# Kernel optimization log

Measured on AMD Instinct MI355X. Metric: run time of the kernel, lower is better.

## Reference

```python
import jax, jax.numpy as jnp
import numpy as np

T, B, I, H = 8192, 1, 1024, 1024


def _lstm_layer(x, W_ih, W_hh, b_ih, b_hh):
    # x: [T, B, I]; torch gate order: input, forget, cell(g), output
    Hh = W_hh.shape[1]
    xg = jnp.einsum('tbi,gi->tbg', x, W_ih) + b_ih + b_hh  # [T, B, 4H]

    def step(carry, xg_t):
        h, c = carry
        gates = xg_t + h @ W_hh.T  # [B, 4H]
        i, f, g, o = jnp.split(gates, 4, axis=-1)
        c = jax.nn.sigmoid(f) * c + jax.nn.sigmoid(i) * jnp.tanh(g)
        h = jax.nn.sigmoid(o) * jnp.tanh(c)
        return (h, c), h

    h0 = jnp.zeros((x.shape[1], Hh), x.dtype)
    (_, _), ys = jax.lax.scan(step, (h0, h0), xg)
    return ys  # [T, B, H]


def setup_inputs() -> dict:
    key = jax.random.key(0)
    ks = jax.random.split(key, 9)
    s = 0.02
    return {
        'inputs': jax.random.normal(ks[0], (T, B, I), dtype=jnp.float32),
        'W_ih0': jax.random.normal(ks[1], (4 * H, I), dtype=jnp.float32) * s,
        'W_hh0': jax.random.normal(ks[2], (4 * H, H), dtype=jnp.float32) * s,
        'b_ih0': jax.random.normal(ks[3], (4 * H,), dtype=jnp.float32) * s,
        'b_hh0': jax.random.normal(ks[4], (4 * H,), dtype=jnp.float32) * s,
        'W_ih1': jax.random.normal(ks[5], (4 * H, H), dtype=jnp.float32) * s,
        'W_hh1': jax.random.normal(ks[6], (4 * H, H), dtype=jnp.float32) * s,
        'b_ih1': jax.random.normal(ks[7], (4 * H,), dtype=jnp.float32) * s,
        'b_hh1': jax.random.normal(ks[8], (4 * H,), dtype=jnp.float32) * s,
    }


def reference(inputs, W_ih0, W_hh0, b_ih0, b_hh0, W_ih1, W_hh1, b_ih1, b_hh1):
    # 2-layer LSTM, zero initial state, dropout omitted (eval semantics)
    y0 = _lstm_layer(inputs, W_ih0, W_hh0, b_ih0, b_hh0)
    y1 = _lstm_layer(y0, W_ih1, W_hh1, b_ih1, b_hh1)
    return y1[-1]  # [B, H] — last timestep of top layer
```

## Files before the change

kernel.cpp:

```cpp
#include <hip/hip_runtime.h>

#define T_STEPS 8192
#define HID 1024
#define G4 4096
#define NBLK 128
#define NTHR 512

typedef unsigned long long ull;
typedef unsigned int uint32;

struct Comm {
    uint32 hA[4][HID];
    uint32 hB[4][HID];
};

__device__ inline float sigm(float x) { return 1.0f / (1.0f + __expf(-x)); }
__device__ inline float tanh_f(float x) {
    x = fminf(fmaxf(x, -15.f), 15.f);
    float e = __expf(-2.0f * x);
    return (1.0f - e) / (1.0f + e);
}
__device__ inline uint32 tagf(float f, uint32 tg) {
    union { float f; uint32 u; } a; a.f = f;
    return (a.u & ~15u) | tg;
}

__global__ __launch_bounds__(256)
void gemm_xg(const float* __restrict__ A, const float* __restrict__ W,
             const float* __restrict__ bi, const float* __restrict__ bh,
             float* __restrict__ out)
{
    __shared__ float As[16][65];
    __shared__ float Bs[16][65];
    const int tid = threadIdx.x;
    const int m0 = blockIdx.y * 64, n0 = blockIdx.x * 64;
    const int tm = tid & 15, tn = tid >> 4;
    const int row = tid >> 2, q = tid & 3;
    float acc[4][4] = {{0.f}};
    for (int k0 = 0; k0 < HID; k0 += 16) {
        float4 a = *(const float4*)(A + (size_t)(m0 + row) * HID + k0 + q * 4);
        float4 b = *(const float4*)(W + (size_t)(n0 + row) * HID + k0 + q * 4);
        __syncthreads();
        As[q*4+0][row] = a.x; As[q*4+1][row] = a.y; As[q*4+2][row] = a.z; As[q*4+3][row] = a.w;
        Bs[q*4+0][row] = b.x; Bs[q*4+1][row] = b.y; Bs[q*4+2][row] = b.z; Bs[q*4+3][row] = b.w;
        __syncthreads();
#pragma unroll
        for (int kk = 0; kk < 16; ++kk) {
            float av[4], bv[4];
#pragma unroll
            for (int i = 0; i < 4; ++i) { av[i] = As[kk][tm*4+i]; bv[i] = Bs[kk][tn*4+i]; }
#pragma unroll
            for (int i = 0; i < 4; ++i)
#pragma unroll
                for (int j = 0; j < 4; ++j) acc[i][j] += av[i] * bv[j];
        }
    }
#pragma unroll
    for (int i = 0; i < 4; ++i) {
        int m = m0 + tm * 4 + i;
#pragma unroll
        for (int j = 0; j < 4; ++j) {
            int n = n0 + tn * 4 + j;
            float v = acc[i][j] + bi[n] + bh[n];
            int jd = n & (HID - 1), gate = n >> 10;
            out[(size_t)m * G4 + (jd >> 3) * 32 + (jd & 7) * 4 + gate] = v;
        }
    }
}

__device__ inline void poll_gather(const uint32* __restrict__ buf, uint32 tg,
                                   int lane, float* __restrict__ lds)
{
    uint32 v[16];
    for (;;) {
        bool ok = true;
#pragma unroll
        for (int r = 0; r < 16; ++r)
            v[r] = __hip_atomic_load(&buf[lane + 64 * r],
                                     __ATOMIC_RELAXED, __HIP_MEMORY_SCOPE_AGENT);
#pragma unroll
        for (int r = 0; r < 16; ++r) ok &= ((v[r] & 15u) == tg);
        if (__all(ok)) break;
    }
#pragma unroll
    for (int r = 0; r < 16; ++r) {
        union { uint32 u; float f; } c; c.u = v[r];
        lds[lane + 64 * r] = c.f;
    }
}

__global__ __launch_bounds__(NTHR)
void lstm_fused(const float* __restrict__ Whh0, const float* __restrict__ xg,
                const float* __restrict__ Wih1, const float* __restrict__ Whh1,
                const float* __restrict__ bih1, const float* __restrict__ bhh1,
                float* __restrict__ outF, Comm* __restrict__ cm)
{
    __shared__ float Wl[32 * HID];
    __shared__ float hlA[HID];
    __shared__ float hlB[HID];
    const int blk = blockIdx.x, tid = threadIdx.x;
    const int wave = tid >> 6, lane = tid & 63;

    if (blk < NBLK) {
        const int k = blk;
#pragma unroll
        for (int i = 0; i < 16; ++i) {
            int l = i * NTHR + tid;
            int r = l >> 8, c = l & 255;
            int w = r >> 2, g = r & 3;
            ((float4*)(Wl + r * HID))[c] =
                ((const float4*)(Whh0 + (size_t)(g * HID + 8 * k + w) * HID))[c];
        }
        for (int i = tid; i < HID; i += NTHR) hlA[i] = 0.f;
        float c_state = 0.f;
        float nx0 = 0.f, nx1 = 0.f, nx2 = 0.f, nx3 = 0.f;
        if (lane == 0) {
            const float* xp = xg + (size_t)0 * G4 + k * 32 + wave * 4;
            nx0 = xp[0]; nx1 = xp[1]; nx2 = xp[2]; nx3 = xp[3];
        }
        __syncthreads();

        for (int t = 0; t < T_STEPS; ++t) {
            float x0 = nx0, x1 = nx1, x2 = nx2, x3 = nx3;
            if (lane == 0 && t + 1 < T_STEPS) {
                const float* xp = xg + (size_t)(t + 1) * G4 + k * 32 + wave * 4;
                nx0 = xp[0]; nx1 = xp[1]; nx2 = xp[2]; nx3 = xp[3];
            }
            float a0 = 0.f, a1 = 0.f, a2 = 0.f, a3 = 0.f;
            const float* wb = Wl + wave * 4 * HID;
#pragma unroll 4
            for (int u = 0; u < 16; ++u) {
                float hv = hlA[u * 64 + lane];
                a0 += wb[0 * HID + u * 64 + lane] * hv;
                a1 += wb[1 * HID + u * 64 + lane] * hv;
                a2 += wb[2 * HID + u * 64 + lane] * hv;
                a3 += wb[3 * HID + u * 64 + lane] * hv;
            }
#pragma unroll
            for (int off = 32; off > 0; off >>= 1) {
                a0 += __shfl_xor(a0, off, 64);
                a1 += __shfl_xor(a1, off, 64);
                a2 += __shfl_xor(a2, off, 64);
                a3 += __shfl_xor(a3, off, 64);
            }
            if (lane == 0) {
                float ig = sigm(x0 + a0);
                float fg = sigm(x1 + a1);
                float gg = tanh_f(x2 + a2);
                float og = sigm(x3 + a3);
                c_state = fg * c_state + ig * gg;
                float h = og * tanh_f(c_state);
                __hip_atomic_store(&cm->hA[t & 3][8 * k + wave],
                                   tagf(h, (t >> 2) & 15),
                                   __ATOMIC_RELAXED, __HIP_MEMORY_SCOPE_AGENT);
            }
            if (t == T_STEPS - 1) break;
            __syncthreads();
            if (wave == 0) {
                poll_gather(cm->hA[t & 3], (t >> 2) & 15, lane, hlA);
            } else if (wave == 1 && t >= 3) {
                const int s = t - 3;
                const uint32 tg = (s >> 2) & 15;
                const uint32* hb = cm->hB[s & 3];
                for (;;) {
                    uint32 b0 = __hip_atomic_load(&hb[8 * lane],
                                                  __ATOMIC_RELAXED, __HIP_MEMORY_SCOPE_AGENT);
                    uint32 b1 = __hip_atomic_load(&hb[8 * (lane + 64)],
                                                  __ATOMIC_RELAXED, __HIP_MEMORY_SCOPE_AGENT);
                    if (__all(((b0 & 15u) == tg) & ((b1 & 15u) == tg))) break;
                }
            }
            __syncthreads();
        }
    } else {
        const int kk = blk - NBLK;
        const int j = 8 * kk + wave;
#pragma unroll
        for (int i = 0; i < 16; ++i) {
            int l = i * NTHR + tid;
            int r = l >> 8, c = l & 255;
            int w = r >> 2, g = r & 3;
            ((float4*)(Wl + r * HID))[c] =
                ((const float4*)(Whh1 + (size_t)(g * HID + 8 * kk + w) * HID))[c];
        }
        float wreg[4][16];
#pragma unroll
        for (int g = 0; g < 4; ++g)
#pragma unroll
            for (int u = 0; u < 16; ++u)
                wreg[g][u] = Wih1[(size_t)(g * HID + j) * HID + u * 64 + lane];
        float bia[4];
#pragma unroll
        for (int g = 0; g < 4; ++g)
            bia[g] = bih1[g * HID + j] + bhh1[g * HID + j];
        for (int i = tid; i < HID; i += NTHR) hlB[i] = 0.f;
        float c_state = 0.f;
        __syncthreads();

        for (int t = 0; t < T_STEPS; ++t) {
            if (wave == 0) {
                poll_gather(cm->hA[t & 3], (t >> 2) & 15, lane, hlA);
            } else if (wave == 1 && t >= 1) {
                const int s = t - 1;
                poll_gather(cm->hB[s & 3], (s >> 2) & 15, lane, hlB);
            }
            __syncthreads();
            float a0 = 0.f, a1 = 0.f, a2 = 0.f, a3 = 0.f;
            const float* wb = Wl + wave * 4 * HID;
#pragma unroll
            for (int u = 0; u < 16; ++u) {
                float h0v = hlA[u * 64 + lane];
                float h1v = hlB[u * 64 + lane];
                a0 += wb[0 * HID + u * 64 + lane] * h1v + wreg[0][u] * h0v;
                a1 += wb[1 * HID + u * 64 + lane] * h1v + wreg[1][u] * h0v;
                a2 += wb[2 * HID + u * 64 + lane] * h1v + wreg[2][u] * h0v;
                a3 += wb[3 * HID + u * 64 + lane] * h1v + wreg[3][u] * h0v;
            }
#pragma unroll
            for (int off = 32; off > 0; off >>= 1) {
                a0 += __shfl_xor(a0, off, 64);
                a1 += __shfl_xor(a1, off, 64);
                a2 += __shfl_xor(a2, off, 64);
                a3 += __shfl_xor(a3, off, 64);
            }
            if (lane == 0) {
                float ig = sigm(bia[0] + a0);
                float fg = sigm(bia[1] + a1);
                float gg = tanh_f(bia[2] + a2);
                float og = sigm(bia[3] + a3);
                c_state = fg * c_state + ig * gg;
                float h = og * tanh_f(c_state);
                if (t == T_STEPS - 1) {
                    outF[j] = h;
                } else {
                    __hip_atomic_store(&cm->hB[t & 3][j],
                                       tagf(h, (t >> 2) & 15),
                                       __ATOMIC_RELAXED, __HIP_MEMORY_SCOPE_AGENT);
                }
            }
            if (t == T_STEPS - 1) break;
            __syncthreads();
        }
    }
}

extern "C" void kernel_launch(void* const* d_in, const int* in_sizes, int n_in,
                              void* d_out, int out_size, void* d_ws, size_t ws_size,
                              hipStream_t stream)
{
    const float* x    = (const float*)d_in[0];
    const float* Wih0 = (const float*)d_in[1];
    const float* Whh0 = (const float*)d_in[2];
    const float* bih0 = (const float*)d_in[3];
    const float* bhh0 = (const float*)d_in[4];
    const float* Wih1 = (const float*)d_in[5];
    const float* Whh1 = (const float*)d_in[6];
    const float* bih1 = (const float*)d_in[7];
    const float* bhh1 = (const float*)d_in[8];

    char* ws = (char*)d_ws;
    float* xg = (float*)ws;
    Comm*  cm = (Comm*)(ws + 134217728);

    (void)hipMemsetAsync(ws + 134217728, 0xFF, sizeof(Comm), stream);

    dim3 gg(G4 / 64, T_STEPS / 64);
    gemm_xg<<<gg, 256, 0, stream>>>(x, Wih0, bih0, bhh0, xg);
    lstm_fused<<<2 * NBLK, NTHR, 0, stream>>>(Whh0, xg, Wih1, Whh1, bih1, bhh1,
                                              (float*)d_out, cm);
}
```

Baseline: 41.64 ms.

## Replace block barriers with per-chunk LDS flags and streamed polling in fused LSTM

Removes the two __syncthreads per timestep in both layer blocks and replaces them with fine-grained workgroup-scope flags. Polling now publishes each 64-element chunk of h to LDS as soon as it arrives, so compute waves can start on early chunks. It also double-buffers the h LDS arrays, widens the global ring to 8 slots with progress counters for backpressure, and interleaves W in LDS so each lane reads one float4 per column. The cost is more spin-waiting on LDS flags and more complex memory-ordering logic, which risks subtle races or livelock.

```diff
diff --git a/kernel.cpp b/kernel.cpp
--- a/kernel.cpp
+++ b/kernel.cpp
@@ -5,13 +5,13 @@
 #define G4 4096
 #define NBLK 128
 #define NTHR 512
-
-typedef unsigned long long ull;
+#define NSLOT 8
+
 typedef unsigned int uint32;
 
 struct Comm {
-    uint32 hA[4][HID];
-    uint32 hB[4][HID];
+    uint32 hA[NSLOT][HID];
+    uint32 hB[NSLOT][HID];
 };
 
 __device__ inline float sigm(float x) { return 1.0f / (1.0f + __expf(-x)); }
@@ -68,24 +68,33 @@
     }
 }
 
-__device__ inline void poll_gather(const uint32* __restrict__ buf, uint32 tg,
-                                   int lane, float* __restrict__ lds)
+#define LD_WG  __HIP_MEMORY_SCOPE_WORKGROUP
+#define LD_AG  __HIP_MEMORY_SCOPE_AGENT
+
+__device__ inline void poll_stream(const uint32* __restrict__ buf, uint32 tg,
+                                   int lane, float* __restrict__ lds,
+                                   int* __restrict__ flags, int fval)
 {
     uint32 v[16];
-    for (;;) {
-        bool ok = true;
+    unsigned pending = 0xFFFFu;
+    while (pending) {
 #pragma unroll
         for (int r = 0; r < 16; ++r)
-            v[r] = __hip_atomic_load(&buf[lane + 64 * r],
-                                     __ATOMIC_RELAXED, __HIP_MEMORY_SCOPE_AGENT);
-#pragma unroll
-        for (int r = 0; r < 16; ++r) ok &= ((v[r] & 15u) == tg);
-        if (__all(ok)) break;
-    }
-#pragma unroll
-    for (int r = 0; r < 16; ++r) {
-        union { uint32 u; float f; } c; c.u = v[r];
-        lds[lane + 64 * r] = c.f;
+            if (pending & (1u << r))
+                v[r] = __hip_atomic_load(&buf[r * 64 + lane], __ATOMIC_RELAXED, LD_AG);
+        unsigned np = pending;
+#pragma unroll
+        for (int r = 0; r < 16; ++r) {
+            if (!(pending & (1u << r))) continue;
+            if (__all((v[r] & 15u) == tg)) {
+                union { uint32 u; float f; } c; c.u = v[r];
+                lds[r * 64 + lane] = c.f;
+                if (lane == 0)
+                    __hip_atomic_store(&flags[r], fval, __ATOMIC_RELEASE, LD_WG);
+                np &= ~(1u << r);
+            }
+        }
+        pending = np;
     }
 }
 
@@ -95,46 +104,62 @@
                 const float* __restrict__ bih1, const float* __restrict__ bhh1,
                 float* __restrict__ outF, Comm* __restrict__ cm)
 {
-    __shared__ float Wl[32 * HID];
-    __shared__ float hlA[HID];
-    __shared__ float hlB[HID];
+    __shared__ float Wl[8 * HID * 4];
+    __shared__ float hlA[2][HID];
+    __shared__ float hlB[2][HID];
+    __shared__ int flagA[2][16];
+    __shared__ int flagB[2][16];
+    __shared__ int prog[8];
+    __shared__ int bpOK;
     const int blk = blockIdx.x, tid = threadIdx.x;
     const int wave = tid >> 6, lane = tid & 63;
-
-    if (blk < NBLK) {
-        const int k = blk;
+    const int kb = (blk < NBLK) ? blk : blk - NBLK;
+
+    if (tid < 16) { flagA[0][tid] = -2; flagA[1][tid] = -1;
+                    flagB[0][tid] = -2; flagB[1][tid] = -1; }
+    if (tid < 8) prog[tid] = -1;
+    if (tid == 0) bpOK = -1;
+    for (int i = tid; i < HID; i += NTHR) {
+        hlA[0][i] = 0.f; hlA[1][i] = 0.f; hlB[0][i] = 0.f; hlB[1][i] = 0.f;
+    }
+    {
+        const float* Wsrc = (blk < NBLK) ? Whh0 : Whh1;
 #pragma unroll
         for (int i = 0; i < 16; ++i) {
             int l = i * NTHR + tid;
-            int r = l >> 8, c = l & 255;
+            int r = l >> 8, c4 = l & 255;
             int w = r >> 2, g = r & 3;
-            ((float4*)(Wl + r * HID))[c] =
-                ((const float4*)(Whh0 + (size_t)(g * HID + 8 * k + w) * HID))[c];
-        }
-        for (int i = tid; i < HID; i += NTHR) hlA[i] = 0.f;
+            float4 v = ((const float4*)(Wsrc + (size_t)(g * HID + 8 * kb + w) * HID))[c4];
+            float* dst = Wl + ((size_t)w * HID + c4 * 4) * 4 + g;
+            dst[0] = v.x; dst[4] = v.y; dst[8] = v.z; dst[12] = v.w;
+        }
+    }
+
+    if (blk < NBLK) {
+        const int k = kb;
         float c_state = 0.f;
         float nx0 = 0.f, nx1 = 0.f, nx2 = 0.f, nx3 = 0.f;
         if (lane == 0) {
-            const float* xp = xg + (size_t)0 * G4 + k * 32 + wave * 4;
+            const float* xp = xg + k * 32 + wave * 4;
             nx0 = xp[0]; nx1 = xp[1]; nx2 = xp[2]; nx3 = xp[3];
         }
         __syncthreads();
 
         for (int t = 0; t < T_STEPS; ++t) {
+            const int pm = (t - 1) & 1;
             float x0 = nx0, x1 = nx1, x2 = nx2, x3 = nx3;
             if (lane == 0 && t + 1 < T_STEPS) {
                 const float* xp = xg + (size_t)(t + 1) * G4 + k * 32 + wave * 4;
                 nx0 = xp[0]; nx1 = xp[1]; nx2 = xp[2]; nx3 = xp[3];
             }
             float a0 = 0.f, a1 = 0.f, a2 = 0.f, a3 = 0.f;
-            const float* wb = Wl + wave * 4 * HID;
-#pragma unroll 4
+            const float* wb = Wl + (size_t)wave * HID * 4;
+#pragma unroll
             for (int u = 0; u < 16; ++u) {
-                float hv = hlA[u * 64 + lane];
-                a0 += wb[0 * HID + u * 64 + lane] * hv;
-                a1 += wb[1 * HID + u * 64 + lane] * hv;
-                a2 += wb[2 * HID + u * 64 + lane] * hv;
-                a3 += wb[3 * HID + u * 64 + lane] * hv;
+                while (__hip_atomic_load(&flagA[pm][u], __ATOMIC_ACQUIRE, LD_WG) != t - 1) {}
+                float hv = hlA[pm][u * 64 + lane];
+                float4 wv = *(const float4*)(wb + (u * 64 + lane) * 4);
+                a0 += wv.x * hv; a1 += wv.y * hv; a2 += wv.z * hv; a3 += wv.w * hv;
             }
 #pragma unroll
             for (int off = 32; off > 0; off >>= 1) {
@@ -143,6 +168,7 @@
                 a2 += __shfl_xor(a2, off, 64);
                 a3 += __shfl_xor(a3, off, 64);
             }
+            while (__hip_atomic_load(&bpOK, __ATOMIC_RELAXED, LD_WG) < t - 7) {}
             if (lane == 0) {
                 float ig = sigm(x0 + a0);
                 float fg = sigm(x1 + a1);
@@ -150,39 +176,40 @@
                 float og = sigm(x3 + a3);
                 c_state = fg * c_state + ig * gg;
                 float h = og * tanh_f(c_state);
-                __hip_atomic_store(&cm->hA[t & 3][8 * k + wave],
-                                   tagf(h, (t >> 2) & 15),
-                                   __ATOMIC_RELAXED, __HIP_MEMORY_SCOPE_AGENT);
+                __hip_atomic_store(&cm->hA[t & 7][8 * k + wave],
+                                   tagf(h, (t >> 3) & 15), __ATOMIC_RELAXED, LD_AG);
             }
             if (t == T_STEPS - 1) break;
-            __syncthreads();
+
             if (wave == 0) {
-                poll_gather(cm->hA[t & 3], (t >> 2) & 15, lane, hlA);
-            } else if (wave == 1 && t >= 3) {
-                const int s = t - 3;
-                const uint32 tg = (s >> 2) & 15;
-                const uint32* hb = cm->hB[s & 3];
-                for (;;) {
-                    uint32 b0 = __hip_atomic_load(&hb[8 * lane],
-                                                  __ATOMIC_RELAXED, __HIP_MEMORY_SCOPE_AGENT);
-                    uint32 b1 = __hip_atomic_load(&hb[8 * (lane + 64)],
-                                                  __ATOMIC_RELAXED, __HIP_MEMORY_SCOPE_AGENT);
-                    if (__all(((b0 & 15u) == tg) & ((b1 & 15u) == tg))) break;
+                if (lane < 8)
+                    while (__hip_atomic_load(&prog[lane], __ATOMIC_ACQUIRE, LD_WG) < t - 1) {}
+                poll_stream(cm->hA[t & 7], (t >> 3) & 15, lane, hlA[t & 1], flagA[t & 1], t);
+                if (lane == 0) __hip_atomic_store(&prog[0], t, __ATOMIC_RELEASE, LD_WG);
+            } else if (wave == 1) {
+                if (t >= 6) {
+                    const int s = t - 6;
+                    const uint32 tg = (s >> 3) & 15;
+                    const uint32* hb = cm->hB[s & 7];
+                    uint32 v[16];
+                    for (;;) {
+                        bool ok = true;
+#pragma unroll
+                        for (int r = 0; r < 16; ++r)
+                            v[r] = __hip_atomic_load(&hb[r * 64 + lane], __ATOMIC_RELAXED, LD_AG);
+#pragma unroll
+                        for (int r = 0; r < 16; ++r) ok &= ((v[r] & 15u) == tg);
+                        if (__all(ok)) break;
+                    }
+                    if (lane == 0) __hip_atomic_store(&bpOK, s, __ATOMIC_RELEASE, LD_WG);
                 }
-            }
-            __syncthreads();
+                if (lane == 0) __hip_atomic_store(&prog[1], t, __ATOMIC_RELEASE, LD_WG);
+            } else {
+                if (lane == 0) __hip_atomic_store(&prog[wave], t, __ATOMIC_RELEASE, LD_WG);
+            }
         }
     } else {
-        const int kk = blk - NBLK;
-        const int j = 8 * kk + wave;
-#pragma unroll
-        for (int i = 0; i < 16; ++i) {
-            int l = i * NTHR + tid;
-            int r = l >> 8, c = l & 255;
-            int w = r >> 2, g = r & 3;
-            ((float4*)(Wl + r * HID))[c] =
-                ((const float4*)(Whh1 + (size_t)(g * HID + 8 * kk + w) * HID))[c];
-        }
+        const int j = 8 * kb + wave;
         float wreg[4][16];
 #pragma unroll
         for (int g = 0; g < 4; ++g)
@@ -193,28 +220,36 @@
 #pragma unroll
         for (int g = 0; g < 4; ++g)
             bia[g] = bih1[g * HID + j] + bhh1[g * HID + j];
-        for (int i = tid; i < HID; i += NTHR) hlB[i] = 0.f;
         float c_state = 0.f;
         __syncthreads();
 
         for (int t = 0; t < T_STEPS; ++t) {
+            const int pA = t & 1, pB = (t - 1) & 1;
             if (wave == 0) {
-                poll_gather(cm->hA[t & 3], (t >> 2) & 15, lane, hlA);
+                if (t >= 2 && lane < 8)
+                    while (__hip_atomic_load(&prog[lane], __ATOMIC_ACQUIRE, LD_WG) < t - 2) {}
+                poll_stream(cm->hA[t & 7], (t >> 3) & 15, lane, hlA[pA], flagA[pA], t);
             } else if (wave == 1 && t >= 1) {
-                const int s = t - 1;
-                poll_gather(cm->hB[s & 3], (s >> 2) & 15, lane, hlB);
-            }
-            __syncthreads();
+                if (t >= 3 && lane < 8)
+                    while (__hip_atomic_load(&prog[lane], __ATOMIC_ACQUIRE, LD_WG) < t - 2) {}
+                poll_stream(cm->hB[(t - 1) & 7], ((t - 1) >> 3) & 15, lane,
+                            hlB[pB], flagB[pB], t - 1);
+            }
             float a0 = 0.f, a1 = 0.f, a2 = 0.f, a3 = 0.f;
-            const float* wb = Wl + wave * 4 * HID;
+            const float* wb = Wl + (size_t)wave * HID * 4;
 #pragma unroll
             for (int u = 0; u < 16; ++u) {
-                float h0v = hlA[u * 64 + lane];
-                float h1v = hlB[u * 64 + lane];
-                a0 += wb[0 * HID + u * 64 + lane] * h1v + wreg[0][u] * h0v;
-                a1 += wb[1 * HID + u * 64 + lane] * h1v + wreg[1][u] * h0v;
-                a2 += wb[2 * HID + u * 64 + lane] * h1v + wreg[2][u] * h0v;
-                a3 += wb[3 * HID + u * 64 + lane] * h1v + wreg[3][u] * h0v;
+                while (__hip_atomic_load(&flagB[pB][u], __ATOMIC_ACQUIRE, LD_WG) != t - 1) {}
+                float hv = hlB[pB][u * 64 + lane];
+                float4 wv = *(const float4*)(wb + (u * 64 + lane) * 4);
+                a0 += wv.x * hv; a1 += wv.y * hv; a2 += wv.z * hv; a3 += wv.w * hv;
+            }
+#pragma unroll
+            for (int u = 0; u < 16; ++u) {
+                while (__hip_atomic_load(&flagA[pA][u], __ATOMIC_ACQUIRE, LD_WG) != t) {}
+                float hv = hlA[pA][u * 64 + lane];
+                a0 += wreg[0][u] * hv; a1 += wreg[1][u] * hv;
+                a2 += wreg[2][u] * hv; a3 += wreg[3][u] * hv;
             }
 #pragma unroll
             for (int off = 32; off > 0; off >>= 1) {
@@ -230,16 +265,15 @@
                 float og = sigm(bia[3] + a3);
                 c_state = fg * c_state + ig * gg;
                 float h = og * tanh_f(c_state);
-                if (t == T_STEPS - 1) {
+                if (t == T_STEPS - 1)
                     outF[j] = h;
-                } else {
-                    __hip_atomic_store(&cm->hB[t & 3][j],
-                                       tagf(h, (t >> 2) & 15),
-                                       __ATOMIC_RELAXED, __HIP_MEMORY_SCOPE_AGENT);
-                }
+                else
+                    __hip_atomic_store(&cm->hB[t & 7][j],
+                                       tagf(h, (t >> 3) & 15), __ATOMIC_RELAXED, LD_AG);
             }
             if (t == T_STEPS - 1) break;
-            __syncthreads();
+            if (lane == 0)
+                __hip_atomic_store(&prog[wave], t, __ATOMIC_RELEASE, LD_WG);
         }
     }
 }
```

After: 53.72 ms. 29.0% more time.

## Split h-vector polling across two waves and deepen ring buffer to eight slots

Applied to the files above, without the earlier changes.

The polling and gather of the 1024-entry h vector is now split across two waves (512 entries each) instead of one wave loading 16 values per lane. This is meant to shorten the per-step spin-wait and gather latency on the recurrent critical path. The comm ring grows from 4 to 8 slots, which lets layer 0 run up to 4 steps ahead of layer 1 with the tag scheme adjusted to match. Layer 0's backpressure check now scans the full hB slot instead of sampling 128 entries. The risk is more polling traffic on global memory and extra wavefronts contending for it.

```diff
diff --git a/kernel.cpp b/kernel.cpp
--- a/kernel.cpp
+++ b/kernel.cpp
@@ -5,14 +5,16 @@
 #define G4 4096
 #define NBLK 128
 #define NTHR 512
-
-typedef unsigned long long ull;
+#define NSLOT 8
+
 typedef unsigned int uint32;
 
 struct Comm {
-    uint32 hA[4][HID];
-    uint32 hB[4][HID];
+    uint32 hA[NSLOT][HID];
+    uint32 hB[NSLOT][HID];
 };
+
+#define LD_AG  __HIP_MEMORY_SCOPE_AGENT
 
 __device__ inline float sigm(float x) { return 1.0f / (1.0f + __expf(-x)); }
 __device__ inline float tanh_f(float x) {
@@ -68,24 +70,37 @@
     }
 }
 
-__device__ inline void poll_gather(const uint32* __restrict__ buf, uint32 tg,
-                                   int lane, float* __restrict__ lds)
+__device__ inline void poll8(const uint32* __restrict__ buf, uint32 tg,
+                             int lane, float* __restrict__ lds)
+{
+    uint32 v[8];
+    for (;;) {
+#pragma unroll
+        for (int r = 0; r < 8; ++r)
+            v[r] = __hip_atomic_load(&buf[r * 64 + lane], __ATOMIC_RELAXED, LD_AG);
+        bool ok = true;
+#pragma unroll
+        for (int r = 0; r < 8; ++r) ok &= ((v[r] & 15u) == tg);
+        if (__all(ok)) break;
+    }
+#pragma unroll
+    for (int r = 0; r < 8; ++r) {
+        union { uint32 u; float f; } c; c.u = v[r];
+        lds[r * 64 + lane] = c.f;
+    }
+}
+
+__device__ inline void scan16(const uint32* __restrict__ buf, uint32 tg, int lane)
 {
     uint32 v[16];
     for (;;) {
         bool ok = true;
 #pragma unroll
         for (int r = 0; r < 16; ++r)
-            v[r] = __hip_atomic_load(&buf[lane + 64 * r],
-                                     __ATOMIC_RELAXED, __HIP_MEMORY_SCOPE_AGENT);
+            v[r] = __hip_atomic_load(&buf[r * 64 + lane], __ATOMIC_RELAXED, LD_AG);
 #pragma unroll
         for (int r = 0; r < 16; ++r) ok &= ((v[r] & 15u) == tg);
         if (__all(ok)) break;
-    }
-#pragma unroll
-    for (int r = 0; r < 16; ++r) {
-        union { uint32 u; float f; } c; c.u = v[r];
-        lds[lane + 64 * r] = c.f;
     }
 }
 
@@ -100,22 +115,27 @@
     __shared__ float hlB[HID];
     const int blk = blockIdx.x, tid = threadIdx.x;
     const int wave = tid >> 6, lane = tid & 63;
-
-    if (blk < NBLK) {
-        const int k = blk;
+    const int kb = (blk < NBLK) ? blk : blk - NBLK;
+
+    {
+        const float* Wsrc = (blk < NBLK) ? Whh0 : Whh1;
 #pragma unroll
         for (int i = 0; i < 16; ++i) {
             int l = i * NTHR + tid;
             int r = l >> 8, c = l & 255;
             int w = r >> 2, g = r & 3;
             ((float4*)(Wl + r * HID))[c] =
-                ((const float4*)(Whh0 + (size_t)(g * HID + 8 * k + w) * HID))[c];
-        }
-        for (int i = tid; i < HID; i += NTHR) hlA[i] = 0.f;
+                ((const float4*)(Wsrc + (size_t)(g * HID + 8 * kb + w) * HID))[c];
+        }
+    }
+    for (int i = tid; i < HID; i += NTHR) { hlA[i] = 0.f; hlB[i] = 0.f; }
+
+    if (blk < NBLK) {
+        const int k = kb;
         float c_state = 0.f;
         float nx0 = 0.f, nx1 = 0.f, nx2 = 0.f, nx3 = 0.f;
         if (lane == 0) {
-            const float* xp = xg + (size_t)0 * G4 + k * 32 + wave * 4;
+            const float* xp = xg + k * 32 + wave * 4;
             nx0 = xp[0]; nx1 = xp[1]; nx2 = xp[2]; nx3 = xp[3];
         }
         __syncthreads();
@@ -150,39 +170,22 @@
                 float og = sigm(x3 + a3);
                 c_state = fg * c_state + ig * gg;
                 float h = og * tanh_f(c_state);
-                __hip_atomic_store(&cm->hA[t & 3][8 * k + wave],
-                                   tagf(h, (t >> 2) & 15),
-                                   __ATOMIC_RELAXED, __HIP_MEMORY_SCOPE_AGENT);
+                __hip_atomic_store(&cm->hA[t & 7][8 * k + wave],
+                                   tagf(h, (t >> 3) & 15), __ATOMIC_RELAXED, LD_AG);
             }
             if (t == T_STEPS - 1) break;
             __syncthreads();
             if (wave == 0) {
-                poll_gather(cm->hA[t & 3], (t >> 2) & 15, lane, hlA);
-            } else if (wave == 1 && t >= 3) {
-                const int s = t - 3;
-                const uint32 tg = (s >> 2) & 15;
-                const uint32* hb = cm->hB[s & 3];
-                for (;;) {
-                    uint32 b0 = __hip_atomic_load(&hb[8 * lane],
-                                                  __ATOMIC_RELAXED, __HIP_MEMORY_SCOPE_AGENT);
-                    uint32 b1 = __hip_atomic_load(&hb[8 * (lane + 64)],
-                                                  __ATOMIC_RELAXED, __HIP_MEMORY_SCOPE_AGENT);
-                    if (__all(((b0 & 15u) == tg) & ((b1 & 15u) == tg))) break;
-                }
+                poll8(cm->hA[t & 7], (t >> 3) & 15, lane, hlA);
+            } else if (wave == 1) {
+                poll8(cm->hA[t & 7] + 512, (t >> 3) & 15, lane, hlA + 512);
+            } else if (wave == 2 && t >= 4) {
+                scan16(cm->hB[(t - 4) & 7], ((t - 4) >> 3) & 15, lane);
             }
             __syncthreads();
         }
     } else {
-        const int kk = blk - NBLK;
-        const int j = 8 * kk + wave;
-#pragma unroll
-        for (int i = 0; i < 16; ++i) {
-            int l = i * NTHR + tid;
-            int r = l >> 8, c = l & 255;
-            int w = r >> 2, g = r & 3;
-            ((float4*)(Wl + r * HID))[c] =
-                ((const float4*)(Whh1 + (size_t)(g * HID + 8 * kk + w) * HID))[c];
-        }
+        const int j = 8 * kb + wave;
         float wreg[4][16];
 #pragma unroll
         for (int g = 0; g < 4; ++g)
@@ -193,16 +196,18 @@
 #pragma unroll
         for (int g = 0; g < 4; ++g)
             bia[g] = bih1[g * HID + j] + bhh1[g * HID + j];
-        for (int i = tid; i < HID; i += NTHR) hlB[i] = 0.f;
         float c_state = 0.f;
         __syncthreads();
 
         for (int t = 0; t < T_STEPS; ++t) {
             if (wave == 0) {
-                poll_gather(cm->hA[t & 3], (t >> 2) & 15, lane, hlA);
-            } else if (wave == 1 && t >= 1) {
-                const int s = t - 1;
-                poll_gather(cm->hB[s & 3], (s >> 2) & 15, lane, hlB);
+                poll8(cm->hA[t & 7], (t >> 3) & 15, lane, hlA);
+            } else if (wave == 1) {
+                poll8(cm->hA[t & 7] + 512, (t >> 3) & 15, lane, hlA + 512);
+            } else if (wave == 2 && t >= 1) {
+                poll8(cm->hB[(t - 1) & 7], ((t - 1) >> 3) & 15, lane, hlB);
+            } else if (wave == 3 && t >= 1) {
+                poll8(cm->hB[(t - 1) & 7] + 512, ((t - 1) >> 3) & 15, lane, hlB + 512);
             }
             __syncthreads();
             float a0 = 0.f, a1 = 0.f, a2 = 0.f, a3 = 0.f;
@@ -230,13 +235,11 @@
                 float og = sigm(bia[3] + a3);
                 c_state = fg * c_state + ig * gg;
                 float h = og * tanh_f(c_state);
-                if (t == T_STEPS - 1) {
+                if (t == T_STEPS - 1)
                     outF[j] = h;
-                } else {
-                    __hip_atomic_store(&cm->hB[t & 3][j],
-                                       tagf(h, (t >> 2) & 15),
-                                       __ATOMIC_RELAXED, __HIP_MEMORY_SCOPE_AGENT);
-                }
+                else
+                    __hip_atomic_store(&cm->hB[t & 7][j],
+                                       tagf(h, (t >> 3) & 15), __ATOMIC_RELAXED, LD_AG);
             }
             if (t == T_STEPS - 1) break;
             __syncthreads();
```

Result: faster. 36.23 ms (-13.0%).
